# Kernel tuning notes

Measured on AMD Instinct MI355X. Metric: run time of the kernel, lower is better.

## Reference

```python
import jax, jax.numpy as jnp
import numpy as np

MASK_VAL = -50000.0
N_HEADS = 16

def setup_inputs() -> dict:
    key = jax.random.key(0)
    k1, k2, k3, k4 = jax.random.split(key, 4)
    b, n, d = 2, 2048, 1024
    s = d ** -0.5  # xavier-ish scale for weights
    return {
        "x": jax.random.normal(k1, (b, n, d), dtype=jnp.float32),
        "Wq": jax.random.normal(k2, (d, d), dtype=jnp.float32) * s,
        "Wkv": jax.random.normal(k3, (d, 2 * d), dtype=jnp.float32) * s,
        "Wo": jax.random.normal(k4, (d, d), dtype=jnp.float32) * s,
    }

def reference(x, Wq, Wkv, Wo):
    b, n, d = x.shape
    h = N_HEADS
    hd = d // h
    scale = hd ** -0.5
    # in-projection
    q = x @ Wq                      # [b, n, d]
    kv = x @ Wkv                    # [b, n, 2d]
    k, v = jnp.split(kv, 2, axis=-1)
    # split heads: b n (h d) -> b h n d
    split = lambda t: t.reshape(b, n, h, hd).transpose(0, 2, 1, 3)
    q, k, v = split(q), split(k), split(v)
    # scaled dot-product scores
    dots = jnp.einsum('bhid,bhjd->bhij', q * scale, k)  # [b, h, n, n]
    # causal mask: upper triangle (j > i) set to MASK_VAL (not -inf, per source)
    causal = jnp.triu(jnp.ones((n, n), dtype=bool), 1)
    dots = jnp.where(causal, MASK_VAL, dots)
    attn = jax.nn.softmax(dots, axis=-1)
    out = jnp.einsum('bhij,bhjd->bhid', attn, v)
    out = out.transpose(0, 2, 1, 3).reshape(b, n, d)  # merge heads
    return out @ Wo
```

## Files before the change

kernel.cpp:

```cpp
#include <hip/hip_runtime.h>
#include <stdint.h>
#include <stddef.h>


typedef __bf16 bf16;
typedef __bf16 bf16x8 __attribute__((ext_vector_type(8)));
typedef __bf16 bf16x4 __attribute__((ext_vector_type(4)));
typedef __bf16 bf16x2 __attribute__((ext_vector_type(2)));
typedef float  f32x4  __attribute__((ext_vector_type(4)));
typedef float  f32x16 __attribute__((ext_vector_type(16)));

#define NSEQ 2048
#define DM   1024
#define HD   64
#define QKVS 3072
#define LOG2E 1.44269504f

#define GLD16(g, l) __builtin_amdgcn_global_load_lds(                         \
    (const __attribute__((address_space(1))) void*)(g),                       \
    (__attribute__((address_space(3))) void*)(l), 16, 0, 0)

__global__ void detect_dtype(const uint32_t* __restrict__ x, int* __restrict__ flag) {
  __shared__ int cnt;
  if (threadIdx.x == 0) cnt = 0;
  __syncthreads();
  int c = 0;
  for (int i = threadIdx.x; i < 4096; i += 256) {
    uint32_t e = (x[i] >> 7) & 0xFF;
    if (e >= 110 && e <= 132) c++;
  }
  atomicAdd(&cnt, c);
  __syncthreads();
  if (threadIdx.x == 0) *flag = (cnt > 2048) ? 1 : 0;
}

__global__ __launch_bounds__(256) void convert_x(
    const void* __restrict__ in, bf16* __restrict__ out, int n,
    const int* __restrict__ flagp) {
  const int flag = *flagp;
  const int i = (blockIdx.x * 256 + threadIdx.x) * 8;
  if (i >= n) return;
  if (flag) {
    *(bf16x8*)(out + i) = *(const bf16x8*)((const bf16*)in + i);
  } else {
    const float* f = (const float*)in;
    bf16x8 v;
#pragma unroll
    for (int e = 0; e < 8; ++e) v[e] = (bf16)f[i + e];
    *(bf16x8*)(out + i) = v;
  }
}

__global__ void transpose_conv(const void* __restrict__ in, bf16* __restrict__ out,
                               int K, int N, const int* __restrict__ flagp) {
  __shared__ bf16 tile[32][33];
  const int flag = *flagp;
  const int k0 = blockIdx.y * 32, n0 = blockIdx.x * 32;
  const int tx = threadIdx.x, ty = threadIdx.y;
  if (flag) {
    const bf16* p = (const bf16*)in;
#pragma unroll
    for (int i = ty; i < 32; i += 8)
      tile[i][tx] = p[(size_t)(k0 + i) * N + n0 + tx];
  } else {
    const float* p = (const float*)in;
#pragma unroll
    for (int i = ty; i < 32; i += 8)
      tile[i][tx] = (bf16)p[(size_t)(k0 + i) * N + n0 + tx];
  }
  __syncthreads();
#pragma unroll
  for (int i = ty; i < 32; i += 8)
    out[(size_t)(n0 + i) * K + k0 + tx] = tile[tx][i];
}

__global__ __launch_bounds__(256) void gemm_bt(
    const bf16* __restrict__ A, const bf16* __restrict__ Bt,
    void* __restrict__ C, int M, int N, int K, const int* flagp)
{
  __shared__ bf16 As[128][64];
  __shared__ bf16 Bs[128][64];
  const int tid  = threadIdx.x;
  const int wave = tid >> 6, lane = tid & 63;
  const int fr = lane & 15, fg = lane >> 4;
  const int m0 = blockIdx.y * 128, n0 = blockIdx.x * 128;
  const int wr = (wave >> 1) * 64, wc = (wave & 1) * 64;
  const int lrow = lane >> 3;
  const int lcol = 8 * ((lane & 7) ^ lrow);

  f32x4 acc[4][4] = {};

  for (int kt = 0; kt < K; kt += 64) {
    __syncthreads();
#pragma unroll
    for (int p = 0; p < 4; ++p) {
      const int chunk = wave * 4 + p;
      const int r = chunk * 8 + lrow;
      GLD16(A  + (size_t)(m0 + r) * K + kt + lcol, &As[chunk * 8][0]);
      GLD16(Bt + (size_t)(n0 + r) * K + kt + lcol, &Bs[chunk * 8][0]);
    }
    __syncthreads();
#pragma unroll
    for (int s = 0; s < 2; ++s) {
      bf16x8 af[4], bfr[4];
#pragma unroll
      for (int i = 0; i < 4; ++i) {
        const int ar = wr + i * 16 + fr;
        af[i]  = *(const bf16x8*)((const char*)&As[ar][0] +
                   ((s * 64 + fg * 16) ^ ((ar & 7) << 4)));
        const int br = wc + i * 16 + fr;
        bfr[i] = *(const bf16x8*)((const char*)&Bs[br][0] +
                   ((s * 64 + fg * 16) ^ ((br & 7) << 4)));
      }
#pragma unroll
      for (int i = 0; i < 4; ++i)
#pragma unroll
        for (int j = 0; j < 4; ++j)
          acc[i][j] = __builtin_amdgcn_mfma_f32_16x16x32_bf16(
              af[i], bfr[j], acc[i][j], 0, 0, 0);
    }
  }
  const int crow = m0 + wr + fg * 4;
  const int ccol = n0 + wc + fr;
  const int as_bf16 = flagp ? *flagp : 1;
  if (as_bf16) {
    bf16* Cb = (bf16*)C;
#pragma unroll
    for (int i = 0; i < 4; ++i)
#pragma unroll
      for (int j = 0; j < 4; ++j)
#pragma unroll
        for (int r = 0; r < 4; ++r)
          Cb[(size_t)(crow + i * 16 + r) * N + ccol + j * 16] = (bf16)acc[i][j][r];
  } else {
    float* Cf = (float*)C;
#pragma unroll
    for (int i = 0; i < 4; ++i)
#pragma unroll
      for (int j = 0; j < 4; ++j)
#pragma unroll
        for (int r = 0; r < 4; ++r)
          Cf[(size_t)(crow + i * 16 + r) * N + ccol + j * 16] = acc[i][j][r];
  }
}

static __device__ inline uint32_t pk2(float a, float b) {
  bf16x2 t; t[0] = (bf16)a; t[1] = (bf16)b;
  return __builtin_bit_cast(uint32_t, t);
}

static __device__ __forceinline__ void strip_compute(
    const bf16x8 (&kf)[2][4], const bf16x8 (&vf)[2][2][2],
    const bf16x8 (&qf)[4], f32x16 (&oacc)[2], float& m, float& l,
    const int j0, const int q0, const int c, const int h)
{
  const int qrow = q0 + c;
  const int blkmax = (j0 + 32 <= q0 + 31) ? 2 : 1;

  f32x16 sv[2];
  __builtin_amdgcn_s_setprio(1);
#pragma unroll
  for (int blk = 0; blk < 2; ++blk)
    if (blk < blkmax) {
      f32x16 a = {};
#pragma unroll
      for (int ks = 0; ks < 4; ++ks)
        a = __builtin_amdgcn_mfma_f32_32x32x16_bf16(kf[blk][ks], qf[ks], a, 0, 0, 0);
      sv[blk] = a;
    }
  __builtin_amdgcn_s_setprio(0);

  if (j0 + 63 > q0) {
#pragma unroll
    for (int blk = 0; blk < 2; ++blk)
      if (blk < blkmax) {
        const int kvb = j0 + blk * 32 + 4 * h;
#pragma unroll
        for (int r = 0; r < 16; ++r) {
          const int kv = kvb + (r & 3) + 8 * (r >> 2);
          if (kv > qrow) sv[blk][r] = -4.0e8f;
        }
      }
  }

  float red[8];
#pragma unroll
  for (int i = 0; i < 8; ++i) {
    float a = fmaxf(sv[0][i], sv[0][i + 8]);
    if (blkmax == 2) a = fmaxf(a, fmaxf(sv[1][i], sv[1][i + 8]));
    red[i] = a;
  }
#pragma unroll
  for (int w = 4; w >= 1; w >>= 1)
#pragma unroll
    for (int i = 0; i < w; ++i) red[i] = fmaxf(red[i], red[i + w]);
  float tmax = red[0];
  tmax = fmaxf(tmax, __shfl_xor(tmax, 32));
  const float pmax = tmax * 0.125f;
  if (!__all(pmax - m <= 8.0f)) {
    const float mnew  = fmaxf(m, pmax);
    const float alpha = __builtin_amdgcn_exp2f((m - mnew) * LOG2E);
    m = mnew;
    l *= alpha;
#pragma unroll
    for (int db = 0; db < 2; ++db)
#pragma unroll
      for (int r = 0; r < 16; ++r) oacc[db][r] *= alpha;
  }
  const float km = 0.125f * LOG2E, kb = -m * LOG2E;
#pragma unroll
  for (int blk = 0; blk < 2; ++blk)
    if (blk < blkmax)
#pragma unroll
      for (int r = 0; r < 16; ++r)
        sv[blk][r] = __builtin_amdgcn_exp2f(__builtin_fmaf(sv[blk][r], km, kb));
  float sr[8];
#pragma unroll
  for (int i = 0; i < 8; ++i) {
    float a = sv[0][i] + sv[0][i + 8];
    if (blkmax == 2) a += sv[1][i] + sv[1][i + 8];
    sr[i] = a;
  }
#pragma unroll
  for (int w = 4; w >= 1; w >>= 1)
#pragma unroll
    for (int i = 0; i < w; ++i) sr[i] += sr[i + w];
  float sum = sr[0];
  sum += __shfl_xor(sum, 32);
  l += sum;

#pragma unroll
  for (int blk = 0; blk < 2; ++blk)
    if (blk < blkmax) {
      uint32_t w[8], xw[8];
#pragma unroll
      for (int g = 0; g < 4; ++g) {
        w[2 * g]     = pk2(sv[blk][4 * g],     sv[blk][4 * g + 1]);
        w[2 * g + 1] = pk2(sv[blk][4 * g + 2], sv[blk][4 * g + 3]);
      }
#pragma unroll
      for (int i = 0; i < 8; ++i)
        xw[i] = (uint32_t)__shfl_xor((int)w[i], 32);
#pragma unroll
      for (int ks = 0; ks < 2; ++ks) {
        union { uint32_t u[4]; bf16x8 v; } pf;
        pf.u[0] = h ? xw[4 * ks + 2] : w[4 * ks];
        pf.u[1] = h ? xw[4 * ks + 3] : w[4 * ks + 1];
        pf.u[2] = h ? w[4 * ks + 2]  : xw[4 * ks];
        pf.u[3] = h ? w[4 * ks + 3]  : xw[4 * ks + 1];
        __builtin_amdgcn_s_setprio(1);
#pragma unroll
        for (int db = 0; db < 2; ++db)
          oacc[db] = __builtin_amdgcn_mfma_f32_32x32x16_bf16(
              vf[blk][ks][db], pf.v, oacc[db], 0, 0, 0);
        __builtin_amdgcn_s_setprio(0);
      }
    }
}

__global__ __launch_bounds__(128) void attn_fwd(
    const bf16* __restrict__ QKV, bf16* __restrict__ O)
{
  __shared__ bf16 Ks[2][64][64];
  __shared__ bf16 Vt[2][64][64];

  const int pr = blockIdx.x;
  const int bh = blockIdx.y;
  const int bi = bh >> 4, hi = bh & 15;
  const int tid = threadIdx.x, wave = tid >> 6, lane = tid & 63;
  const int c = lane & 31, h = lane >> 5;

  const bf16* qptr = QKV + (size_t)bi * NSEQ * QKVS + hi * HD;
  const bf16* kptr = qptr + DM;
  const bf16* vptr = qptr + 2 * DM;

  const int sA = 2 * pr + wave, sB = 63 - sA;
  const int q0A = sA * 32, q0B = sB * 32;

  bf16x8 qfA[4], qfB[4];
#pragma unroll
  for (int ks = 0; ks < 4; ++ks) {
    qfA[ks] = *(const bf16x8*)(qptr + (size_t)(q0A + c) * QKVS + ks * 16 + h * 8);
    qfB[ks] = *(const bf16x8*)(qptr + (size_t)(q0B + c) * QKVS + ks * 16 + h * 8);
  }

  f32x16 oaccA[2] = {}, oaccB[2] = {};
  float mA = -1e30f, lA = 0.f, mB = -1e30f, lB = 0.f;

  const int srow = tid >> 3, sch = tid & 7;
  const int koff = (sch * 16) ^ ((srow & 7) << 4);
  const int kvg = (tid & 15) * 4, dg = (tid >> 4) * 8;

  bf16x8 kpre[4], vpre[4];

  const int ntil = 32 - pr;

  {
#pragma unroll
    for (int p = 0; p < 4; ++p)
      kpre[p] = *(const bf16x8*)(kptr + (size_t)(srow + 16 * p) * QKVS + sch * 8);
#pragma unroll
    for (int i = 0; i < 4; ++i)
      vpre[i] = *(const bf16x8*)(vptr + (size_t)(kvg + i) * QKVS + dg);
#pragma unroll
    for (int p = 0; p < 4; ++p)
      *(bf16x8*)((char*)&Ks[0][srow + 16 * p][0] + koff) = kpre[p];
#pragma unroll
    for (int e = 0; e < 8; ++e) {
      const int d = dg + e;
      bf16x4 w; w[0] = vpre[0][e]; w[1] = vpre[1][e];
      w[2] = vpre[2][e]; w[3] = vpre[3][e];
      *(bf16x4*)((char*)&Vt[0][d][0] + ((2 * kvg) ^ ((d & 7) << 4))) = w;
    }
#pragma unroll
    for (int p = 0; p < 4; ++p)
      kpre[p] = *(const bf16x8*)(kptr + (size_t)(64 + srow + 16 * p) * QKVS + sch * 8);
#pragma unroll
    for (int i = 0; i < 4; ++i)
      vpre[i] = *(const bf16x8*)(vptr + (size_t)(64 + kvg + i) * QKVS + dg);
  }
  __syncthreads();

  for (int t = 0; t < ntil; ++t) {
    const int cur = t & 1;
    const int j0 = t * 64;

    if (t + 1 < ntil) {
      const int nb = cur ^ 1;
#pragma unroll
      for (int p = 0; p < 4; ++p)
        *(bf16x8*)((char*)&Ks[nb][srow + 16 * p][0] + koff) = kpre[p];
#pragma unroll
      for (int e = 0; e < 8; ++e) {
        const int d = dg + e;
        bf16x4 w; w[0] = vpre[0][e]; w[1] = vpre[1][e];
        w[2] = vpre[2][e]; w[3] = vpre[3][e];
        *(bf16x4*)((char*)&Vt[nb][d][0] + ((2 * kvg) ^ ((d & 7) << 4))) = w;
      }
    }
    if (t + 2 < ntil) {
      const int jn = j0 + 128;
#pragma unroll
      for (int p = 0; p < 4; ++p)
        kpre[p] = *(const bf16x8*)(kptr + (size_t)(jn + srow + 16 * p) * QKVS + sch * 8);
#pragma unroll
      for (int i = 0; i < 4; ++i)
        vpre[i] = *(const bf16x8*)(vptr + (size_t)(jn + kvg + i) * QKVS + dg);
    }

    bf16x8 kf[2][4], vf[2][2][2];
#pragma unroll
    for (int blk = 0; blk < 2; ++blk) {
      const int krow = blk * 32 + c;
#pragma unroll
      for (int ks = 0; ks < 4; ++ks)
        kf[blk][ks] = *(const bf16x8*)((const char*)&Ks[cur][krow][0] +
                       ((ks * 32 + h * 16) ^ ((krow & 7) << 4)));
#pragma unroll
      for (int ks = 0; ks < 2; ++ks)
#pragma unroll
        for (int db = 0; db < 2; ++db) {
          const int vrow = db * 32 + c;
          vf[blk][ks][db] = *(const bf16x8*)((const char*)&Vt[cur][vrow][0] +
                             ((blk * 64 + ks * 32 + h * 16) ^ ((vrow & 7) << 4)));
        }
    }

    strip_compute(kf, vf, qfB, oaccB, mB, lB, j0, q0B, c, h);
    if (j0 <= q0A + 31)
      strip_compute(kf, vf, qfA, oaccA, mA, lA, j0, q0A, c, h);

    __syncthreads();
  }

#pragma unroll
  for (int sidx = 0; sidx < 2; ++sidx) {
    const f32x16* oacc = sidx ? oaccB : oaccA;
    const float linv = 1.f / (sidx ? lB : lA);
    const int q0 = sidx ? q0B : q0A;
    bf16* obase = O + (size_t)bi * NSEQ * DM + (size_t)hi * HD +
                  (size_t)(q0 + c) * DM;
#pragma unroll
    for (int db = 0; db < 2; ++db)
#pragma unroll
      for (int g = 0; g < 4; ++g) {
        bf16x4 ov;
#pragma unroll
        for (int j = 0; j < 4; ++j) ov[j] = (bf16)(oacc[db][4 * g + j] * linv);
        *(bf16x4*)(obase + db * 32 + 8 * g + 4 * h) = ov;
      }
  }
}

extern "C" void kernel_launch(void* const* d_in, const int* in_sizes, int n_in,
                              void* d_out, int out_size, void* d_ws, size_t ws_size,
                              hipStream_t stream) {
  const void* x   = d_in[0];
  const void* Wq  = d_in[1];
  const void* Wkv = d_in[2];
  const void* Wo  = d_in[3];

  char* ws = (char*)d_ws;
  int*  flag   = (int*)ws;
  bf16* xb     = (bf16*)(ws + (4ull << 10));
  bf16* WqkvT  = (bf16*)(ws + (4ull << 10) + (8ull  << 20));
  bf16* WoT    = (bf16*)(ws + (4ull << 10) + (14ull << 20));
  bf16* QKVb   = (bf16*)(ws + (4ull << 10) + (16ull << 20));
  bf16* AOb    = xb;

  detect_dtype<<<1, 256, 0, stream>>>((const uint32_t*)x, flag);
  convert_x<<<4194304 / 8 / 256, 256, 0, stream>>>(x, xb, 4194304, flag);

  const dim3 tb(32, 8);
  transpose_conv<<<dim3(1024 / 32, 1024 / 32), tb, 0, stream>>>(Wq,  WqkvT,                1024, 1024, flag);
  transpose_conv<<<dim3(2048 / 32, 1024 / 32), tb, 0, stream>>>(Wkv, WqkvT + 1024 * 1024,  1024, 2048, flag);
  transpose_conv<<<dim3(1024 / 32, 1024 / 32), tb, 0, stream>>>(Wo,  WoT,                  1024, 1024, flag);

  gemm_bt<<<dim3(3072 / 128, 4096 / 128), 256, 0, stream>>>(xb, WqkvT, QKVb, 4096, 3072, 1024, nullptr);

  attn_fwd<<<dim3(16, 32), 128, 0, stream>>>(QKVb, AOb);

  gemm_bt<<<dim3(1024 / 128, 4096 / 128), 256, 0, stream>>>(AOb, WoT, d_out, 4096, 1024, 1024, flag);
}
```

Measured before the change: 150.7 us.

## Split KV tiles across two wave groups in attention and merge partial softmax

Doubles attention block size to four waves, where two wave groups each own alternating KV tiles with separate double-buffered LDS staging. At the end, partial output accumulators, row max and row sum from one group are passed through LDS and merged with the other using rescaled exponentials. This aims to raise wave-level parallelism and latency hiding for the small attention grid, at the cost of doubled LDS use and an extra merge step.

```diff
diff --git a/kernel.cpp b/kernel.cpp
--- a/kernel.cpp
+++ b/kernel.cpp
@@ -258,24 +258,26 @@
     }
 }
 
-__global__ __launch_bounds__(128) void attn_fwd(
+__global__ __launch_bounds__(256) void attn_fwd(
     const bf16* __restrict__ QKV, bf16* __restrict__ O)
 {
-  __shared__ bf16 Ks[2][64][64];
-  __shared__ bf16 Vt[2][64][64];
-
-  const int pr = blockIdx.x;
+  __shared__ bf16 Ks[2][2][64][64];
+  __shared__ bf16 Vt[2][2][64][64];
+
+  const int bx = blockIdx.x;
   const int bh = blockIdx.y;
   const int bi = bh >> 4, hi = bh & 15;
   const int tid = threadIdx.x, wave = tid >> 6, lane = tid & 63;
   const int c = lane & 31, h = lane >> 5;
+  const int pq = wave & 1;
+  const int z  = wave >> 1;
 
   const bf16* qptr = QKV + (size_t)bi * NSEQ * QKVS + hi * HD;
   const bf16* kptr = qptr + DM;
   const bf16* vptr = qptr + 2 * DM;
 
-  const int sA = 2 * pr + wave, sB = 63 - sA;
-  const int q0A = sA * 32, q0B = sB * 32;
+  const int p = 2 * bx + pq;
+  const int q0A = p * 32, q0B = (63 - p) * 32;
 
   bf16x8 qfA[4], qfB[4];
 #pragma unroll
@@ -287,108 +289,140 @@
   f32x16 oaccA[2] = {}, oaccB[2] = {};
   float mA = -1e30f, lA = 0.f, mB = -1e30f, lB = 0.f;
 
-  const int srow = tid >> 3, sch = tid & 7;
-  const int koff = (sch * 16) ^ ((srow & 7) << 4);
-  const int kvg = (tid & 15) * 4, dg = (tid >> 4) * 8;
+  const int ht = tid & 127;
+  const int hsrow = ht >> 3, hsch = ht & 7;
+  const int hkoff = (hsch * 16) ^ ((hsrow & 7) << 4);
+  const int hkvg = (ht & 15) * 4, hdg = (ht >> 4) * 8;
 
   bf16x8 kpre[4], vpre[4];
 
-  const int ntil = 32 - pr;
+  const int ntil = 32 - bx;
+  const int niter = (ntil + 1) >> 1;
 
   {
-#pragma unroll
-    for (int p = 0; p < 4; ++p)
-      kpre[p] = *(const bf16x8*)(kptr + (size_t)(srow + 16 * p) * QKVS + sch * 8);
+    const size_t jz = (size_t)(z * 64);
+#pragma unroll
+    for (int pp = 0; pp < 4; ++pp)
+      kpre[pp] = *(const bf16x8*)(kptr + (jz + hsrow + 16 * pp) * QKVS + hsch * 8);
 #pragma unroll
     for (int i = 0; i < 4; ++i)
-      vpre[i] = *(const bf16x8*)(vptr + (size_t)(kvg + i) * QKVS + dg);
-#pragma unroll
-    for (int p = 0; p < 4; ++p)
-      *(bf16x8*)((char*)&Ks[0][srow + 16 * p][0] + koff) = kpre[p];
+      vpre[i] = *(const bf16x8*)(vptr + (jz + hkvg + i) * QKVS + hdg);
+#pragma unroll
+    for (int pp = 0; pp < 4; ++pp)
+      *(bf16x8*)((char*)&Ks[z][0][hsrow + 16 * pp][0] + hkoff) = kpre[pp];
 #pragma unroll
     for (int e = 0; e < 8; ++e) {
-      const int d = dg + e;
+      const int d = hdg + e;
       bf16x4 w; w[0] = vpre[0][e]; w[1] = vpre[1][e];
       w[2] = vpre[2][e]; w[3] = vpre[3][e];
-      *(bf16x4*)((char*)&Vt[0][d][0] + ((2 * kvg) ^ ((d & 7) << 4))) = w;
-    }
-#pragma unroll
-    for (int p = 0; p < 4; ++p)
-      kpre[p] = *(const bf16x8*)(kptr + (size_t)(64 + srow + 16 * p) * QKVS + sch * 8);
-#pragma unroll
-    for (int i = 0; i < 4; ++i)
-      vpre[i] = *(const bf16x8*)(vptr + (size_t)(64 + kvg + i) * QKVS + dg);
+      *(bf16x4*)((char*)&Vt[z][0][d][0] + ((2 * hkvg) ^ ((d & 7) << 4))) = w;
+    }
+    if (z + 2 < ntil) {
+      const size_t jn = (size_t)((z + 2) * 64);
+#pragma unroll
+      for (int pp = 0; pp < 4; ++pp)
+        kpre[pp] = *(const bf16x8*)(kptr + (jn + hsrow + 16 * pp) * QKVS + hsch * 8);
+#pragma unroll
+      for (int i = 0; i < 4; ++i)
+        vpre[i] = *(const bf16x8*)(vptr + (jn + hkvg + i) * QKVS + hdg);
+    }
   }
   __syncthreads();
 
-  for (int t = 0; t < ntil; ++t) {
-    const int cur = t & 1;
-    const int j0 = t * 64;
-
-    if (t + 1 < ntil) {
-      const int nb = cur ^ 1;
-#pragma unroll
-      for (int p = 0; p < 4; ++p)
-        *(bf16x8*)((char*)&Ks[nb][srow + 16 * p][0] + koff) = kpre[p];
+  for (int i = 0; i < niter; ++i) {
+    const int cur = i & 1;
+
+    if (2 * i + 2 + z < ntil) {
+#pragma unroll
+      for (int pp = 0; pp < 4; ++pp)
+        *(bf16x8*)((char*)&Ks[z][cur ^ 1][hsrow + 16 * pp][0] + hkoff) = kpre[pp];
 #pragma unroll
       for (int e = 0; e < 8; ++e) {
-        const int d = dg + e;
+        const int d = hdg + e;
         bf16x4 w; w[0] = vpre[0][e]; w[1] = vpre[1][e];
         w[2] = vpre[2][e]; w[3] = vpre[3][e];
-        *(bf16x4*)((char*)&Vt[nb][d][0] + ((2 * kvg) ^ ((d & 7) << 4))) = w;
-      }
-    }
-    if (t + 2 < ntil) {
-      const int jn = j0 + 128;
-#pragma unroll
-      for (int p = 0; p < 4; ++p)
-        kpre[p] = *(const bf16x8*)(kptr + (size_t)(jn + srow + 16 * p) * QKVS + sch * 8);
-#pragma unroll
-      for (int i = 0; i < 4; ++i)
-        vpre[i] = *(const bf16x8*)(vptr + (size_t)(jn + kvg + i) * QKVS + dg);
-    }
-
-    bf16x8 kf[2][4], vf[2][2][2];
-#pragma unroll
-    for (int blk = 0; blk < 2; ++blk) {
-      const int krow = blk * 32 + c;
-#pragma unroll
-      for (int ks = 0; ks < 4; ++ks)
-        kf[blk][ks] = *(const bf16x8*)((const char*)&Ks[cur][krow][0] +
-                       ((ks * 32 + h * 16) ^ ((krow & 7) << 4)));
-#pragma unroll
-      for (int ks = 0; ks < 2; ++ks)
-#pragma unroll
-        for (int db = 0; db < 2; ++db) {
-          const int vrow = db * 32 + c;
-          vf[blk][ks][db] = *(const bf16x8*)((const char*)&Vt[cur][vrow][0] +
-                             ((blk * 64 + ks * 32 + h * 16) ^ ((vrow & 7) << 4)));
+        *(bf16x4*)((char*)&Vt[z][cur ^ 1][d][0] + ((2 * hkvg) ^ ((d & 7) << 4))) = w;
+      }
+    }
+    if (2 * i + 4 + z < ntil) {
+      const size_t jn = (size_t)((2 * i + 4 + z) * 64);
+#pragma unroll
+      for (int pp = 0; pp < 4; ++pp)
+        kpre[pp] = *(const bf16x8*)(kptr + (jn + hsrow + 16 * pp) * QKVS + hsch * 8);
+#pragma unroll
+      for (int ii = 0; ii < 4; ++ii)
+        vpre[ii] = *(const bf16x8*)(vptr + (jn + hkvg + ii) * QKVS + hdg);
+    }
+
+    const int tj = 2 * i + z;
+    if (tj < ntil) {
+      const int j0 = tj * 64;
+      bf16x8 kf[2][4], vf[2][2][2];
+#pragma unroll
+      for (int blk = 0; blk < 2; ++blk) {
+        const int krow = blk * 32 + c;
+#pragma unroll
+        for (int ks = 0; ks < 4; ++ks)
+          kf[blk][ks] = *(const bf16x8*)((const char*)&Ks[z][cur][krow][0] +
+                         ((ks * 32 + h * 16) ^ ((krow & 7) << 4)));
+#pragma unroll
+        for (int ks = 0; ks < 2; ++ks)
+#pragma unroll
+          for (int db = 0; db < 2; ++db) {
+            const int vrow = db * 32 + c;
+            vf[blk][ks][db] = *(const bf16x8*)((const char*)&Vt[z][cur][vrow][0] +
+                               ((blk * 64 + ks * 32 + h * 16) ^ ((vrow & 7) << 4)));
+          }
+      }
+      strip_compute(kf, vf, qfB, oaccB, mB, lB, j0, q0B, c, h);
+      if (j0 <= q0A + 31)
+        strip_compute(kf, vf, qfA, oaccA, mA, lA, j0, q0A, c, h);
+    }
+
+    __syncthreads();
+  }
+
+  float* pbuf = (float*)&Ks[0][0][0][0];
+  if (z == 1) {
+#pragma unroll
+    for (int sidx = 0; sidx < 2; ++sidx) {
+      float* dst = pbuf + ((size_t)((pq * 2 + sidx) * 64 + lane)) * 37;
+      const f32x16* oacc = sidx ? oaccB : oaccA;
+#pragma unroll
+      for (int db = 0; db < 2; ++db)
+#pragma unroll
+        for (int r = 0; r < 16; ++r) dst[db * 16 + r] = oacc[db][r];
+      dst[32] = sidx ? mB : mA;
+      dst[33] = sidx ? lB : lA;
+    }
+  }
+  __syncthreads();
+  if (z == 0) {
+#pragma unroll
+    for (int sidx = 0; sidx < 2; ++sidx) {
+      const float* src = pbuf + ((size_t)((pq * 2 + sidx) * 64 + lane)) * 37;
+      const f32x16* oacc = sidx ? oaccB : oaccA;
+      const float m0v = sidx ? mB : mA, l0v = sidx ? lB : lA;
+      const float m1v = src[32], l1v = src[33];
+      const float M  = fmaxf(m0v, m1v);
+      const float w0 = __builtin_amdgcn_exp2f((m0v - M) * LOG2E);
+      const float w1 = __builtin_amdgcn_exp2f((m1v - M) * LOG2E);
+      const float linv = 1.f / (w0 * l0v + w1 * l1v);
+      const int q0 = sidx ? q0B : q0A;
+      bf16* obase = O + (size_t)bi * NSEQ * DM + (size_t)hi * HD +
+                    (size_t)(q0 + c) * DM;
+#pragma unroll
+      for (int db = 0; db < 2; ++db)
+#pragma unroll
+        for (int g = 0; g < 4; ++g) {
+          bf16x4 ov;
+#pragma unroll
+          for (int j = 0; j < 4; ++j)
+            ov[j] = (bf16)((w0 * oacc[db][4 * g + j] +
+                            w1 * src[db * 16 + 4 * g + j]) * linv);
+          *(bf16x4*)(obase + db * 32 + 8 * g + 4 * h) = ov;
         }
     }
-
-    strip_compute(kf, vf, qfB, oaccB, mB, lB, j0, q0B, c, h);
-    if (j0 <= q0A + 31)
-      strip_compute(kf, vf, qfA, oaccA, mA, lA, j0, q0A, c, h);
-
-    __syncthreads();
-  }
-
-#pragma unroll
-  for (int sidx = 0; sidx < 2; ++sidx) {
-    const f32x16* oacc = sidx ? oaccB : oaccA;
-    const float linv = 1.f / (sidx ? lB : lA);
-    const int q0 = sidx ? q0B : q0A;
-    bf16* obase = O + (size_t)bi * NSEQ * DM + (size_t)hi * HD +
-                  (size_t)(q0 + c) * DM;
-#pragma unroll
-    for (int db = 0; db < 2; ++db)
-#pragma unroll
-      for (int g = 0; g < 4; ++g) {
-        bf16x4 ov;
-#pragma unroll
-        for (int j = 0; j < 4; ++j) ov[j] = (bf16)(oacc[db][4 * g + j] * linv);
-        *(bf16x4*)(obase + db * 32 + 8 * g + 4 * h) = ov;
-      }
   }
 }
 
@@ -418,7 +452,7 @@
 
   gemm_bt<<<dim3(3072 / 128, 4096 / 128), 256, 0, stream>>>(xb, WqkvT, QKVb, 4096, 3072, 1024, nullptr);
 
-  attn_fwd<<<dim3(16, 32), 128, 0, stream>>>(QKVb, AOb);
+  attn_fwd<<<dim3(16, 32), 256, 0, stream>>>(QKVb, AOb);
 
   gemm_bt<<<dim3(1024 / 128, 4096 / 128), 256, 0, stream>>>(AOb, WoT, d_out, 4096, 1024, 1024, flag);
 }
```

Measured after the change: 175.1 us. 1.16x slower.

## Interleave two query strips' QK, softmax and PV stages for ILP

Applied to the files above, without the earlier changes.

When both query strips are active for a KV tile, a new dual_strip_compute interleaves the two strips' QK^T MFMA chains, masking, reductions, exponentials and PV MFMAs instead of running them back to back. The aim is to hide MFMA latency and softmax VALU work behind independent work from the other strip. The s_setprio hints around the MFMAs are also removed. The interleaving raises register pressure by keeping two score tiles live at once, which could cause spills or lower occupancy.

```diff
diff --git a/kernel.cpp b/kernel.cpp
--- a/kernel.cpp
+++ b/kernel.cpp
@@ -149,52 +149,112 @@
   return __builtin_bit_cast(uint32_t, t);
 }
 
+static __device__ __forceinline__ void qkt_chain(
+    const bf16x8 (&kf)[2][4], const bf16x8 (&qf)[4], f32x16 (&sv)[2],
+    const int bm)
+{
+#pragma unroll
+  for (int blk = 0; blk < 2; ++blk)
+    if (blk < bm) {
+      f32x16 a = {};
+#pragma unroll
+      for (int ks = 0; ks < 4; ++ks)
+        a = __builtin_amdgcn_mfma_f32_32x32x16_bf16(kf[blk][ks], qf[ks], a, 0, 0, 0);
+      sv[blk] = a;
+    }
+}
+
+static __device__ __forceinline__ void mask_sv(
+    f32x16 (&sv)[2], const int bm, const int j0, const int qrow, const int h)
+{
+#pragma unroll
+  for (int blk = 0; blk < 2; ++blk)
+    if (blk < bm) {
+      const int kvb = j0 + blk * 32 + 4 * h;
+#pragma unroll
+      for (int r = 0; r < 16; ++r) {
+        const int kv = kvb + (r & 3) + 8 * (r >> 2);
+        if (kv > qrow) sv[blk][r] = -4.0e8f;
+      }
+    }
+}
+
+static __device__ __forceinline__ float tree_max(const f32x16 (&sv)[2], const int bm)
+{
+  float red[8];
+#pragma unroll
+  for (int i = 0; i < 8; ++i) {
+    float a = fmaxf(sv[0][i], sv[0][i + 8]);
+    if (bm == 2) a = fmaxf(a, fmaxf(sv[1][i], sv[1][i + 8]));
+    red[i] = a;
+  }
+#pragma unroll
+  for (int w = 4; w >= 1; w >>= 1)
+#pragma unroll
+    for (int i = 0; i < w; ++i) red[i] = fmaxf(red[i], red[i + w]);
+  return red[0];
+}
+
+static __device__ __forceinline__ float tree_sum(const f32x16 (&sv)[2], const int bm)
+{
+  float sr[8];
+#pragma unroll
+  for (int i = 0; i < 8; ++i) {
+    float a = sv[0][i] + sv[0][i + 8];
+    if (bm == 2) a += sv[1][i] + sv[1][i + 8];
+    sr[i] = a;
+  }
+#pragma unroll
+  for (int w = 4; w >= 1; w >>= 1)
+#pragma unroll
+    for (int i = 0; i < w; ++i) sr[i] += sr[i + w];
+  return sr[0];
+}
+
+static __device__ __forceinline__ void repack_pv(
+    const f32x16 (&sv)[2], const bf16x8 (&vf)[2][2][2], f32x16 (&oacc)[2],
+    const int bm, const int h)
+{
+#pragma unroll
+  for (int blk = 0; blk < 2; ++blk)
+    if (blk < bm) {
+      uint32_t w[8], xw[8];
+#pragma unroll
+      for (int g = 0; g < 4; ++g) {
+        w[2 * g]     = pk2(sv[blk][4 * g],     sv[blk][4 * g + 1]);
+        w[2 * g + 1] = pk2(sv[blk][4 * g + 2], sv[blk][4 * g + 3]);
+      }
+#pragma unroll
+      for (int i = 0; i < 8; ++i)
+        xw[i] = (uint32_t)__shfl_xor((int)w[i], 32);
+#pragma unroll
+      for (int ks = 0; ks < 2; ++ks) {
+        union { uint32_t u[4]; bf16x8 v; } pf;
+        pf.u[0] = h ? xw[4 * ks + 2] : w[4 * ks];
+        pf.u[1] = h ? xw[4 * ks + 3] : w[4 * ks + 1];
+        pf.u[2] = h ? w[4 * ks + 2]  : xw[4 * ks];
+        pf.u[3] = h ? w[4 * ks + 3]  : xw[4 * ks + 1];
+#pragma unroll
+        for (int db = 0; db < 2; ++db)
+          oacc[db] = __builtin_amdgcn_mfma_f32_32x32x16_bf16(
+              vf[blk][ks][db], pf.v, oacc[db], 0, 0, 0);
+      }
+    }
+}
+
 static __device__ __forceinline__ void strip_compute(
     const bf16x8 (&kf)[2][4], const bf16x8 (&vf)[2][2][2],
     const bf16x8 (&qf)[4], f32x16 (&oacc)[2], float& m, float& l,
     const int j0, const int q0, const int c, const int h)
 {
   const int qrow = q0 + c;
-  const int blkmax = (j0 + 32 <= q0 + 31) ? 2 : 1;
+  const int bm = (j0 + 32 <= q0 + 31) ? 2 : 1;
 
   f32x16 sv[2];
-  __builtin_amdgcn_s_setprio(1);
-#pragma unroll
-  for (int blk = 0; blk < 2; ++blk)
-    if (blk < blkmax) {
-      f32x16 a = {};
-#pragma unroll
-      for (int ks = 0; ks < 4; ++ks)
-        a = __builtin_amdgcn_mfma_f32_32x32x16_bf16(kf[blk][ks], qf[ks], a, 0, 0, 0);
-      sv[blk] = a;
-    }
-  __builtin_amdgcn_s_setprio(0);
-
-  if (j0 + 63 > q0) {
-#pragma unroll
-    for (int blk = 0; blk < 2; ++blk)
-      if (blk < blkmax) {
-        const int kvb = j0 + blk * 32 + 4 * h;
-#pragma unroll
-        for (int r = 0; r < 16; ++r) {
-          const int kv = kvb + (r & 3) + 8 * (r >> 2);
-          if (kv > qrow) sv[blk][r] = -4.0e8f;
-        }
-      }
-  }
-
-  float red[8];
-#pragma unroll
-  for (int i = 0; i < 8; ++i) {
-    float a = fmaxf(sv[0][i], sv[0][i + 8]);
-    if (blkmax == 2) a = fmaxf(a, fmaxf(sv[1][i], sv[1][i + 8]));
-    red[i] = a;
-  }
-#pragma unroll
-  for (int w = 4; w >= 1; w >>= 1)
-#pragma unroll
-    for (int i = 0; i < w; ++i) red[i] = fmaxf(red[i], red[i + w]);
-  float tmax = red[0];
+  qkt_chain(kf, qf, sv, bm);
+  if (j0 + 63 > q0) mask_sv(sv, bm, j0, qrow, h);
+
+  float tmax = tree_max(sv, bm);
   tmax = fmaxf(tmax, __shfl_xor(tmax, 32));
   const float pmax = tmax * 0.125f;
   if (!__all(pmax - m <= 8.0f)) {
@@ -210,52 +270,132 @@
   const float km = 0.125f * LOG2E, kb = -m * LOG2E;
 #pragma unroll
   for (int blk = 0; blk < 2; ++blk)
-    if (blk < blkmax)
+    if (blk < bm)
 #pragma unroll
       for (int r = 0; r < 16; ++r)
         sv[blk][r] = __builtin_amdgcn_exp2f(__builtin_fmaf(sv[blk][r], km, kb));
-  float sr[8];
-#pragma unroll
-  for (int i = 0; i < 8; ++i) {
-    float a = sv[0][i] + sv[0][i + 8];
-    if (blkmax == 2) a += sv[1][i] + sv[1][i + 8];
-    sr[i] = a;
-  }
-#pragma unroll
-  for (int w = 4; w >= 1; w >>= 1)
-#pragma unroll
-    for (int i = 0; i < w; ++i) sr[i] += sr[i + w];
-  float sum = sr[0];
+  float sum = tree_sum(sv, bm);
   sum += __shfl_xor(sum, 32);
   l += sum;
 
-#pragma unroll
-  for (int blk = 0; blk < 2; ++blk)
-    if (blk < blkmax) {
-      uint32_t w[8], xw[8];
+  repack_pv(sv, vf, oacc, bm, h);
+}
+
+static __device__ __forceinline__ void dual_strip_compute(
+    const bf16x8 (&kf)[2][4], const bf16x8 (&vf)[2][2][2],
+    const bf16x8 (&qfA)[4], const bf16x8 (&qfB)[4],
+    f32x16 (&oaccA)[2], f32x16 (&oaccB)[2],
+    float& mA, float& lA, float& mB, float& lB,
+    const int j0, const int q0A, const int q0B, const int c, const int h)
+{
+  const int qrowA = q0A + c, qrowB = q0B + c;
+  const int bmA = (j0 + 32 <= q0A + 31) ? 2 : 1;
+  const int bmB = (j0 + 32 <= q0B + 31) ? 2 : 1;
+
+  f32x16 svA[2], svB[2];
+  qkt_chain(kf, qfB, svB, bmB);
+  qkt_chain(kf, qfA, svA, bmA);
+
+  if (j0 + 63 > q0B) mask_sv(svB, bmB, j0, qrowB, h);
+  if (j0 + 63 > q0A) mask_sv(svA, bmA, j0, qrowA, h);
+
+  float tmaxB = tree_max(svB, bmB);
+  float tmaxA = tree_max(svA, bmA);
+  tmaxB = fmaxf(tmaxB, __shfl_xor(tmaxB, 32));
+  tmaxA = fmaxf(tmaxA, __shfl_xor(tmaxA, 32));
+  const float pmaxB = tmaxB * 0.125f, pmaxA = tmaxA * 0.125f;
+  if (!__all(pmaxB - mB <= 8.0f)) {
+    const float mnew  = fmaxf(mB, pmaxB);
+    const float alpha = __builtin_amdgcn_exp2f((mB - mnew) * LOG2E);
+    mB = mnew;
+    lB *= alpha;
+#pragma unroll
+    for (int db = 0; db < 2; ++db)
+#pragma unroll
+      for (int r = 0; r < 16; ++r) oaccB[db][r] *= alpha;
+  }
+  if (!__all(pmaxA - mA <= 8.0f)) {
+    const float mnew  = fmaxf(mA, pmaxA);
+    const float alpha = __builtin_amdgcn_exp2f((mA - mnew) * LOG2E);
+    mA = mnew;
+    lA *= alpha;
+#pragma unroll
+    for (int db = 0; db < 2; ++db)
+#pragma unroll
+      for (int r = 0; r < 16; ++r) oaccA[db][r] *= alpha;
+  }
+  const float km = 0.125f * LOG2E;
+  const float kbB = -mB * LOG2E, kbA = -mA * LOG2E;
+#pragma unroll
+  for (int blk = 0; blk < 2; ++blk) {
+    if (blk < bmB)
+#pragma unroll
+      for (int r = 0; r < 16; ++r)
+        svB[blk][r] = __builtin_amdgcn_exp2f(__builtin_fmaf(svB[blk][r], km, kbB));
+    if (blk < bmA)
+#pragma unroll
+      for (int r = 0; r < 16; ++r)
+        svA[blk][r] = __builtin_amdgcn_exp2f(__builtin_fmaf(svA[blk][r], km, kbA));
+  }
+  float sumB = tree_sum(svB, bmB);
+  float sumA = tree_sum(svA, bmA);
+  sumB += __shfl_xor(sumB, 32);
+  sumA += __shfl_xor(sumA, 32);
+  lB += sumB;
+  lA += sumA;
+
+#pragma unroll
+  for (int blk = 0; blk < 2; ++blk) {
+    uint32_t wB[8], xwB[8], wA[8], xwA[8];
+    if (blk < bmB) {
 #pragma unroll
       for (int g = 0; g < 4; ++g) {
-        w[2 * g]     = pk2(sv[blk][4 * g],     sv[blk][4 * g + 1]);
-        w[2 * g + 1] = pk2(sv[blk][4 * g + 2], sv[blk][4 * g + 3]);
+        wB[2 * g]     = pk2(svB[blk][4 * g],     svB[blk][4 * g + 1]);
+        wB[2 * g + 1] = pk2(svB[blk][4 * g + 2], svB[blk][4 * g + 3]);
       }
 #pragma unroll
       for (int i = 0; i < 8; ++i)
-        xw[i] = (uint32_t)__shfl_xor((int)w[i], 32);
+        xwB[i] = (uint32_t)__shfl_xor((int)wB[i], 32);
+    }
+    if (blk < bmA) {
+#pragma unroll
+      for (int g = 0; g < 4; ++g) {
+        wA[2 * g]     = pk2(svA[blk][4 * g],     svA[blk][4 * g + 1]);
+        wA[2 * g + 1] = pk2(svA[blk][4 * g + 2], svA[blk][4 * g + 3]);
+      }
+#pragma unroll
+      for (int i = 0; i < 8; ++i)
+        xwA[i] = (uint32_t)__shfl_xor((int)wA[i], 32);
+    }
+    if (blk < bmB) {
 #pragma unroll
       for (int ks = 0; ks < 2; ++ks) {
         union { uint32_t u[4]; bf16x8 v; } pf;
-        pf.u[0] = h ? xw[4 * ks + 2] : w[4 * ks];
-        pf.u[1] = h ? xw[4 * ks + 3] : w[4 * ks + 1];
-        pf.u[2] = h ? w[4 * ks + 2]  : xw[4 * ks];
-        pf.u[3] = h ? w[4 * ks + 3]  : xw[4 * ks + 1];
-        __builtin_amdgcn_s_setprio(1);
+        pf.u[0] = h ? xwB[4 * ks + 2] : wB[4 * ks];
+        pf.u[1] = h ? xwB[4 * ks + 3] : wB[4 * ks + 1];
+        pf.u[2] = h ? wB[4 * ks + 2]  : xwB[4 * ks];
+        pf.u[3] = h ? wB[4 * ks + 3]  : xwB[4 * ks + 1];
 #pragma unroll
         for (int db = 0; db < 2; ++db)
-          oacc[db] = __builtin_amdgcn_mfma_f32_32x32x16_bf16(
-              vf[blk][ks][db], pf.v, oacc[db], 0, 0, 0);
-        __builtin_amdgcn_s_setprio(0);
-      }
-    }
+          oaccB[db] = __builtin_amdgcn_mfma_f32_32x32x16_bf16(
+              vf[blk][ks][db], pf.v, oaccB[db], 0, 0, 0);
+      }
+    }
+    if (blk < bmA) {
+#pragma unroll
+      for (int ks = 0; ks < 2; ++ks) {
+        union { uint32_t u[4]; bf16x8 v; } pf;
+        pf.u[0] = h ? xwA[4 * ks + 2] : wA[4 * ks];
+        pf.u[1] = h ? xwA[4 * ks + 3] : wA[4 * ks + 1];
+        pf.u[2] = h ? wA[4 * ks + 2]  : xwA[4 * ks];
+        pf.u[3] = h ? wA[4 * ks + 3]  : xwA[4 * ks + 1];
+#pragma unroll
+        for (int db = 0; db < 2; ++db)
+          oaccA[db] = __builtin_amdgcn_mfma_f32_32x32x16_bf16(
+              vf[blk][ks][db], pf.v, oaccA[db], 0, 0, 0);
+      }
+    }
+  }
 }
 
 __global__ __launch_bounds__(128) void attn_fwd(
@@ -366,9 +506,11 @@
         }
     }
 
-    strip_compute(kf, vf, qfB, oaccB, mB, lB, j0, q0B, c, h);
     if (j0 <= q0A + 31)
-      strip_compute(kf, vf, qfA, oaccA, mA, lA, j0, q0A, c, h);
+      dual_strip_compute(kf, vf, qfA, qfB, oaccA, oaccB,
+                         mA, lA, mB, lB, j0, q0A, q0B, c, h);
+    else
+      strip_compute(kf, vf, qfB, oaccB, mB, lB, j0, q0B, c, h);
 
     __syncthreads();
   }
```

After: 149.4 us. About the same (-0.9%).
